# Kernel tuning notes

Measured on AMD Instinct MI355X. Metric: run time of the kernel, lower is better.

Reference implementation:

```python
import jax, jax.numpy as jnp
import numpy as np

IMG = 1024.0
POOL = 7
STRIDES = (4, 8, 16, 32)  # levels P2..P5
STDS = jnp.array([0.1, 0.1, 0.2, 0.2], dtype=jnp.float32)  # RCNN_TARGET_STDS


def delta2bbox(rois, deltas):
    # rois: [N,4] (y1,x1,y2,x2) pixels; deltas: [N,4]
    d = deltas * STDS  # means are zero
    y1, x1, y2, x2 = rois[:, 0], rois[:, 1], rois[:, 2], rois[:, 3]
    h = y2 - y1
    w = x2 - x1
    cy = y1 + 0.5 * h + d[:, 0] * h
    cx = x1 + 0.5 * w + d[:, 1] * w
    h = h * jnp.exp(d[:, 2])
    w = w * jnp.exp(d[:, 3])
    b = jnp.stack([cy - 0.5 * h, cx - 0.5 * w, cy + 0.5 * h, cx + 0.5 * w], axis=1)
    return jnp.clip(b, 0.0, IMG)


def crop_level(feat, rois, stride):
    # feat: [H,W,C]; bilinear 7x7 crop (crop_and_resize style)
    H, W, _ = feat.shape
    s = rois / stride
    grid = (jnp.arange(POOL, dtype=jnp.float32) + 0.5) / POOL
    ys = s[:, 0:1] + grid[None, :] * (s[:, 2:3] - s[:, 0:1])  # [N,7]
    xs = s[:, 1:2] + grid[None, :] * (s[:, 3:4] - s[:, 1:2])  # [N,7]
    y0f = jnp.clip(jnp.floor(ys), 0.0, H - 1)
    x0f = jnp.clip(jnp.floor(xs), 0.0, W - 1)
    y0 = y0f.astype(jnp.int32)
    x0 = x0f.astype(jnp.int32)
    y1 = jnp.minimum(y0 + 1, H - 1)
    x1 = jnp.minimum(x0 + 1, W - 1)
    wy = jnp.clip(ys - y0f, 0.0, 1.0)[:, :, None, None]  # [N,7,1,1]
    wx = jnp.clip(xs - x0f, 0.0, 1.0)[:, None, :, None]  # [N,1,7,1]
    g = lambda yi, xi: feat[yi[:, :, None], xi[:, None, :]]  # [N,7,7,C]
    return (g(y0, x0) * (1 - wy) * (1 - wx) + g(y0, x1) * (1 - wy) * wx
            + g(y1, x0) * wy * (1 - wx) + g(y1, x1) * wy * wx)


def pyramid_roi_align(feats, rois):
    h = rois[:, 2] - rois[:, 0]
    w = rois[:, 3] - rois[:, 1]
    lvl = jnp.floor(4.0 + jnp.log2(jnp.sqrt(jnp.maximum(h * w, 1e-6)) / 224.0))
    lvl = jnp.clip(lvl, 2.0, 5.0).astype(jnp.int32)
    pooled = 0.0
    for i, (feat, stride) in enumerate(zip(feats, STRIDES)):
        mask = (lvl == i + 2).astype(feat.dtype)[:, None, None, None]
        pooled = pooled + crop_level(feat, rois, stride) * mask
    return pooled  # [N,7,7,C]


def bbox_head(pooled, i, fc1_w, fc1_b, fc2_w, fc2_b, cls_w, cls_b, reg_w, reg_b):
    n = pooled.shape[0]
    x = pooled.reshape(n, -1)
    h1 = jax.nn.relu(x @ fc1_w[i] + fc1_b[i])
    h2 = jax.nn.relu(h1 @ fc2_w[i] + fc2_b[i])
    logits = h2 @ cls_w[i] + cls_b[i]
    probs = jax.nn.softmax(logits, axis=-1)
    deltas = h2 @ reg_w[i] + reg_b[i]
    return logits, probs, deltas


def setup_inputs() -> dict:
    key = jax.random.key(0)
    ks = jax.random.split(key, 16)
    d = {}
    for j, (name, shp) in enumerate([("P2", (1, 256, 256, 256)), ("P3", (1, 128, 128, 256)),
                                     ("P4", (1, 64, 64, 256)), ("P5", (1, 32, 32, 256))]):
        d[name] = jax.random.normal(ks[j], shp, dtype=jnp.float32)
    N = 1000
    u = jax.random.uniform(ks[4], (N, 4))
    hh = 16.0 * 2.0 ** (u[:, 0] * 5.0)  # box sizes 16..512 px, spans all pyramid levels
    ww = 16.0 * 2.0 ** (u[:, 1] * 5.0)
    y1 = u[:, 2] * (IMG - hh)
    x1 = u[:, 3] * (IMG - ww)
    d["rois"] = jnp.stack([y1, x1, y1 + hh, x1 + ww], axis=1)
    d["fc1_w"] = jax.random.normal(ks[5], (3, 12544, 1024), dtype=jnp.float32) * 0.01
    d["fc1_b"] = jnp.zeros((3, 1024), jnp.float32)
    d["fc2_w"] = jax.random.normal(ks[6], (3, 1024, 1024), dtype=jnp.float32) * 0.02
    d["fc2_b"] = jnp.zeros((3, 1024), jnp.float32)
    d["cls_w"] = jax.random.normal(ks[7], (3, 1024, 81), dtype=jnp.float32) * 0.02
    d["cls_b"] = jnp.zeros((3, 81), jnp.float32)
    d["reg_w"] = jax.random.normal(ks[8], (3, 1024, 4), dtype=jnp.float32) * 0.01
    d["reg_b"] = jnp.zeros((3, 4), jnp.float32)
    return d


def reference(P2, P3, P4, P5, rois, fc1_w, fc1_b, fc2_w, fc2_b, cls_w, cls_b, reg_w, reg_b):
    feats = [P2[0], P3[0], P4[0], P5[0]]
    params = (fc1_w, fc1_b, fc2_w, fc2_b, cls_w, cls_b, reg_w, reg_b)
    r = rois
    probs3 = None
    pooled = None
    for i in range(3):
        pooled = pyramid_roi_align(feats, r)
        _, probs3, deltas = bbox_head(pooled, i, *params)
        if i < 2:
            r = delta2bbox(r, deltas)
    # test-time ensemble: heads 1 and 2 re-applied to final pooled regions
    _, probs1, _ = bbox_head(pooled, 0, *params)
    _, probs2, _ = bbox_head(pooled, 1, *params)
    return (probs3 + probs1 + probs2) / 3.0
```

## Files before the change

### kernel.cpp

```cpp
#include <hip/hip_runtime.h>


#define BM 128
#define BN 128
#define BK 32
#define K1 12544
#define MPAD 1024
#define NROI 1000

typedef __bf16 bf16_t;
typedef bf16_t bf16x8 __attribute__((ext_vector_type(8)));
typedef float f32x4 __attribute__((ext_vector_type(4)));
typedef float f32x2 __attribute__((ext_vector_type(2)));
typedef unsigned short u16x4 __attribute__((ext_vector_type(4)));
typedef unsigned short u16x2 __attribute__((ext_vector_type(2)));

__device__ __forceinline__ unsigned short f2bf(float x) {
  unsigned u = __float_as_uint(x);
  return (unsigned short)((u + 0x7fffu + ((u >> 16) & 1u)) >> 16);
}
__device__ __forceinline__ float bf2f(unsigned short h) {
  return __uint_as_float(((unsigned)h) << 16);
}

__device__ __forceinline__ void gld_lds16(const void* g, void* l) {
  __builtin_amdgcn_global_load_lds(
      (__attribute__((address_space(1))) void*)g,
      (__attribute__((address_space(3))) void*)l, 16, 0, 0);
}

template <bool SPLIT>
__global__ __launch_bounds__(256, 4)
void gemm_bf16(const unsigned short* __restrict__ Ah,
               const unsigned short* __restrict__ Al,
               long long strideA_head,
               const unsigned short* __restrict__ Bh,
               const unsigned short* __restrict__ Bl,
               long long strideB_head,
               float* __restrict__ Cpart,
               int Nh, int K, int kcSteps)
{
  __shared__ __align__(16) unsigned short sAh[BM * BK];
  __shared__ __align__(16) unsigned short sBh[BN * BK];
  __shared__ __align__(16) unsigned short sAl[SPLIT ? BM * BK : 8];
  __shared__ __align__(16) unsigned short sBl[SPLIT ? BN * BK : 8];

  const int t = threadIdx.x;
  const int ntile = Nh / BN;
  const int bm = blockIdx.x / ntile;
  const int bn = blockIdx.x % ntile;
  const int s = blockIdx.y;
  const int h = blockIdx.z;
  const int H = gridDim.z;

  const unsigned short* Ab = Ah + (size_t)h * strideA_head + (size_t)bm * BM * K;
  const unsigned short* Bb = Bh + (size_t)h * strideB_head + (size_t)bn * BN * K;
  const unsigned short* Alb = SPLIT ? (Al + (size_t)h * strideA_head + (size_t)bm * BM * K) : (const unsigned short*)0;
  const unsigned short* Blb = SPLIT ? (Bl + (size_t)h * strideB_head + (size_t)bn * BN * K) : (const unsigned short*)0;

  int k0 = s * kcSteps * BK;
  int k1 = min(K, k0 + kcSteps * BK);

  const int srow = t >> 2;
  const int gsw = ((t & 3) ^ ((srow >> 1) & 3)) * 8;
  const int lane = t & 63;
  const int wv = t >> 6;
  const int wm = (wv >> 1) * 64;
  const int wn = (wv & 1) * 64;
  const int lr = lane & 15;
  const int q = lane >> 4;
  const int sw = (lr >> 1) & 3;
  const int cA = (q ^ sw) * 8;

  f32x4 acc[4][4];
  const f32x4 z = {0.f, 0.f, 0.f, 0.f};
#pragma unroll
  for (int i = 0; i < 4; ++i)
#pragma unroll
    for (int j = 0; j < 4; ++j) acc[i][j] = z;

  for (int kk = k0; kk < k1; kk += BK) {
#pragma unroll
    for (int j = 0; j < 2; ++j) {
      int row = j * 64 + srow;
      gld_lds16(Ab + (size_t)row * K + kk + gsw, (char*)sAh + j * 4096 + t * 16);
      gld_lds16(Bb + (size_t)row * K + kk + gsw, (char*)sBh + j * 4096 + t * 16);
      if constexpr (SPLIT) {
        gld_lds16(Alb + (size_t)row * K + kk + gsw, (char*)sAl + j * 4096 + t * 16);
        gld_lds16(Blb + (size_t)row * K + kk + gsw, (char*)sBl + j * 4096 + t * 16);
      }
    }
    __syncthreads();

    bf16x8 af[4], bfr[4];
#pragma unroll
    for (int i = 0; i < 4; ++i) af[i] = *(const bf16x8*)&sAh[(wm + i * 16 + lr) * BK + cA];
#pragma unroll
    for (int j = 0; j < 4; ++j) bfr[j] = *(const bf16x8*)&sBh[(wn + j * 16 + lr) * BK + cA];
#pragma unroll
    for (int i = 0; i < 4; ++i)
#pragma unroll
      for (int j = 0; j < 4; ++j)
        acc[i][j] = __builtin_amdgcn_mfma_f32_16x16x32_bf16(af[i], bfr[j], acc[i][j], 0, 0, 0);

    if constexpr (SPLIT) {
      bf16x8 al[4], bl[4];
#pragma unroll
      for (int i = 0; i < 4; ++i) al[i] = *(const bf16x8*)&sAl[(wm + i * 16 + lr) * BK + cA];
#pragma unroll
      for (int j = 0; j < 4; ++j) bl[j] = *(const bf16x8*)&sBl[(wn + j * 16 + lr) * BK + cA];
#pragma unroll
      for (int i = 0; i < 4; ++i)
#pragma unroll
        for (int j = 0; j < 4; ++j) {
          acc[i][j] = __builtin_amdgcn_mfma_f32_16x16x32_bf16(af[i], bl[j], acc[i][j], 0, 0, 0);
          acc[i][j] = __builtin_amdgcn_mfma_f32_16x16x32_bf16(al[i], bfr[j], acc[i][j], 0, 0, 0);
        }
    }
    __syncthreads();
  }

  float* Cb = Cpart + ((size_t)(s * H + h) * MPAD + (size_t)bm * BM) * Nh + (size_t)bn * BN;
#pragma unroll
  for (int i = 0; i < 4; ++i)
#pragma unroll
    for (int j = 0; j < 4; ++j)
#pragma unroll
      for (int r = 0; r < 4; ++r) {
        int m = wm + i * 16 + q * 4 + r;
        int n = wn + j * 16 + lr;
        Cb[(size_t)m * Nh + n] = acc[i][j][r];
      }
}

__global__ __launch_bounds__(256)
void epilogue_kernel(const float* __restrict__ Cpart, int S, int H, int Nh,
                     const float* __restrict__ bias,
                     unsigned short* __restrict__ ohi,
                     unsigned short* __restrict__ olo, int flags)
{
  size_t total = (size_t)H * MPAD * Nh;
  size_t idx = ((size_t)blockIdx.x * 256 + threadIdx.x) * 4;
  if (idx >= total) return;
  int n = (int)(idx % Nh);
  int h = (int)(idx / ((size_t)MPAD * Nh));
  f32x4 v = *(const f32x4*)&bias[(size_t)h * Nh + n];
  for (int s = 0; s < S; ++s) v += *(const f32x4*)&Cpart[(size_t)s * total + idx];
  u16x4 hi, lo;
#pragma unroll
  for (int j = 0; j < 4; ++j) {
    float x = fmaxf(v[j], 0.f);
    hi[j] = f2bf(x);
    lo[j] = f2bf(x - bf2f(hi[j]));
  }
  *(u16x4*)&ohi[idx] = hi;
  if (flags & 4) *(u16x4*)&olo[idx] = lo;
}

__global__ __launch_bounds__(256)
void transpose_convert(const float* __restrict__ W,
                       unsigned short* __restrict__ Thi,
                       unsigned short* __restrict__ Tlo,
                       int K, int N, int loHeads)
{
  __shared__ float tile[32][260];
  int kb = blockIdx.x * 256;
  int nb = blockIdx.y * 32;
  int h = blockIdx.z;
  const float* Wb = W + (size_t)h * K * N + (size_t)kb * N + nb;
  int tn = threadIdx.x & 31;
  int tk = threadIdx.x >> 5;
#pragma unroll
  for (int i = 0; i < 32; ++i) {
    int k = tk + i * 8;
    tile[tn][k] = Wb[(size_t)k * N + tn];
  }
  __syncthreads();
  bool wlo = h < loHeads;
  int l = threadIdx.x & 63;
  int ng = threadIdx.x >> 6;
  size_t ob = (size_t)h * N * K + (size_t)nb * K + kb;
#pragma unroll
  for (int i = 0; i < 8; ++i) {
    int n = ng + i * 4;
    f32x4 v = *(const f32x4*)&tile[n][4 * l];
    u16x4 hi;
#pragma unroll
    for (int j = 0; j < 4; ++j) hi[j] = f2bf(v[j]);
    *(u16x4*)&Thi[ob + (size_t)n * K + 4 * l] = hi;
    if (wlo) {
      u16x4 lo;
#pragma unroll
      for (int j = 0; j < 4; ++j) lo[j] = f2bf(v[j] - bf2f(hi[j]));
      *(u16x4*)&Tlo[ob + (size_t)n * K + 4 * l] = lo;
    }
  }
}

__global__ void transpose_cls(const float* __restrict__ W, unsigned short* __restrict__ T)
{
  int n = blockIdx.x, h = blockIdx.y, t = threadIdx.x;
  size_t ob = ((size_t)h * 128 + n) * 1024;
  if (n < 81) {
    for (int k = t; k < 1024; k += 256)
      T[ob + k] = f2bf(W[((size_t)h * 1024 + k) * 81 + n]);
  } else {
    for (int k = t; k < 1024; k += 256) T[ob + k] = 0;
  }
}

__global__ void roi_align_kernel(const float* __restrict__ rois,
                                 const float* __restrict__ P2, const float* __restrict__ P3,
                                 const float* __restrict__ P4, const float* __restrict__ P5,
                                 unsigned short* __restrict__ phi,
                                 unsigned short* __restrict__ plo, int writeLo)
{
  int m = blockIdx.x;
  int t = threadIdx.x;
  int c = (t & 127) * 2;
  int pg = t >> 7;
  const float* rp = rois + m * 4;
  float y1 = rp[0], x1 = rp[1], y2 = rp[2], x2 = rp[3];
  float hh = y2 - y1, ww = x2 - x1;
  float a = sqrtf(fmaxf(hh * ww, 1e-6f)) / 224.0f;
  float lvl = floorf(4.0f + log2f(a));
  lvl = fminf(fmaxf(lvl, 2.0f), 5.0f);
  int i = (int)lvl - 2;
  const float* f = (i == 0) ? P2 : (i == 1) ? P3 : (i == 2) ? P4 : P5;
  int H = 256 >> i;
  float stride = (float)(4 << i);
  float sy1 = y1 / stride, sx1 = x1 / stride;
  float dy = y2 / stride - sy1, dx = x2 / stride - sx1;
  size_t base = (size_t)m * K1 + c;
  for (int p = pg; p < 49; p += 2) {
    int py = p / 7, px = p % 7;
    float ys = sy1 + ((py + 0.5f) / 7.0f) * dy;
    float xs = sx1 + ((px + 0.5f) / 7.0f) * dx;
    float y0f = fminf(fmaxf(floorf(ys), 0.0f), (float)(H - 1));
    float x0f = fminf(fmaxf(floorf(xs), 0.0f), (float)(H - 1));
    int y0 = (int)y0f, x0 = (int)x0f;
    int y1i = min(y0 + 1, H - 1), x1i = min(x0 + 1, H - 1);
    float wy = fminf(fmaxf(ys - y0f, 0.0f), 1.0f);
    float wx = fminf(fmaxf(xs - x0f, 0.0f), 1.0f);
    f32x2 v00 = *(const f32x2*)(f + ((size_t)y0 * H + x0) * 256 + c);
    f32x2 v01 = *(const f32x2*)(f + ((size_t)y0 * H + x1i) * 256 + c);
    f32x2 v10 = *(const f32x2*)(f + ((size_t)y1i * H + x0) * 256 + c);
    f32x2 v11 = *(const f32x2*)(f + ((size_t)y1i * H + x1i) * 256 + c);
    float w00 = (1.f - wy) * (1.f - wx), w01 = (1.f - wy) * wx;
    float w10 = wy * (1.f - wx), w11 = wy * wx;
    f32x2 v = v00 * w00 + v01 * w01 + v10 * w10 + v11 * w11;
    u16x2 hi;
    hi[0] = f2bf(v[0]); hi[1] = f2bf(v[1]);
    *(u16x2*)&phi[base + p * 256] = hi;
    if (writeLo) {
      u16x2 lo;
      lo[0] = f2bf(v[0] - bf2f(hi[0]));
      lo[1] = f2bf(v[1] - bf2f(hi[1]));
      *(u16x2*)&plo[base + p * 256] = lo;
    }
  }
}

__global__ void reg_delta_kernel(const float* __restrict__ Cpart, int S,
                                 const float* __restrict__ fb,
                                 const float* __restrict__ rw, const float* __restrict__ rb,
                                 const float* __restrict__ rin, float* __restrict__ rout)
{
  int m = blockIdx.x, t = threadIdx.x;
  float s0 = 0, s1 = 0, s2 = 0, s3 = 0;
  for (int n = t; n < 1024; n += 256) {
    float v = fb[n];
    for (int s = 0; s < S; ++s) v += Cpart[((size_t)s * 1024 + m) * 1024 + n];
    v = fmaxf(v, 0.f);
    const float* w = rw + (size_t)n * 4;
    s0 += v * w[0]; s1 += v * w[1]; s2 += v * w[2]; s3 += v * w[3];
  }
#pragma unroll
  for (int o = 32; o > 0; o >>= 1) {
    s0 += __shfl_xor(s0, o, 64);
    s1 += __shfl_xor(s1, o, 64);
    s2 += __shfl_xor(s2, o, 64);
    s3 += __shfl_xor(s3, o, 64);
  }
  __shared__ float part[4][4];
  int w = t >> 6;
  if ((t & 63) == 0) { part[w][0] = s0; part[w][1] = s1; part[w][2] = s2; part[w][3] = s3; }
  __syncthreads();
  if (t == 0) {
    float d0 = (part[0][0] + part[1][0] + part[2][0] + part[3][0] + rb[0]) * 0.1f;
    float d1 = (part[0][1] + part[1][1] + part[2][1] + part[3][1] + rb[1]) * 0.1f;
    float d2 = (part[0][2] + part[1][2] + part[2][2] + part[3][2] + rb[2]) * 0.2f;
    float d3 = (part[0][3] + part[1][3] + part[2][3] + part[3][3] + rb[3]) * 0.2f;
    const float* r = rin + m * 4;
    float y1 = r[0], x1 = r[1], y2 = r[2], x2 = r[3];
    float h = y2 - y1, wd = x2 - x1;
    float cy = y1 + 0.5f * h + d0 * h;
    float cx = x1 + 0.5f * wd + d1 * wd;
    float nh = h * expf(d2);
    float nw = wd * expf(d3);
    float* ro = rout + m * 4;
    ro[0] = fminf(fmaxf(cy - 0.5f * nh, 0.f), 1024.f);
    ro[1] = fminf(fmaxf(cx - 0.5f * nw, 0.f), 1024.f);
    ro[2] = fminf(fmaxf(cy + 0.5f * nh, 0.f), 1024.f);
    ro[3] = fminf(fmaxf(cx + 0.5f * nw, 0.f), 1024.f);
  }
}

__global__ void softmax_avg_kernel(const float* __restrict__ Cpart, int S,
                                   const float* __restrict__ cls_b,
                                   float* __restrict__ out)
{
  int m = blockIdx.x, t = threadIdx.x;
  __shared__ float sh[128];
  float pacc = 0.0f;
  for (int h = 0; h < 3; ++h) {
    float x = -3.0e38f;
    if (t < 81) {
      x = cls_b[h * 81 + t];
      for (int s = 0; s < S; ++s)
        x += Cpart[((size_t)(s * 3 + h) * 1024 + m) * 128 + t];
    }
    sh[t] = x; __syncthreads();
    for (int o = 64; o > 0; o >>= 1) { if (t < o) sh[t] = fmaxf(sh[t], sh[t + o]); __syncthreads(); }
    float mx = sh[0]; __syncthreads();
    float e = (t < 81) ? expf(x - mx) : 0.0f;
    sh[t] = e; __syncthreads();
    for (int o = 64; o > 0; o >>= 1) { if (t < o) sh[t] += sh[t + o]; __syncthreads(); }
    float sum = sh[0]; __syncthreads();
    pacc += e / sum;
  }
  if (t < 81) out[(size_t)m * 81 + t] = pacc / 3.0f;
}

extern "C" void kernel_launch(void* const* d_in, const int* in_sizes, int n_in,
                              void* d_out, int out_size, void* d_ws, size_t ws_size,
                              hipStream_t stream)
{
  const float* P2 = (const float*)d_in[0];
  const float* P3 = (const float*)d_in[1];
  const float* P4 = (const float*)d_in[2];
  const float* P5 = (const float*)d_in[3];
  const float* rois = (const float*)d_in[4];
  const float* fc1_w = (const float*)d_in[5];
  const float* fc1_b = (const float*)d_in[6];
  const float* fc2_w = (const float*)d_in[7];
  const float* fc2_b = (const float*)d_in[8];
  const float* cls_w = (const float*)d_in[9];
  const float* cls_b = (const float*)d_in[10];
  const float* reg_w = (const float*)d_in[11];
  const float* reg_b = (const float*)d_in[12];
  float* out = (float*)d_out;

  char* ws = (char*)d_ws;
  size_t off = 0;
  auto alloc = [&](size_t b) -> char* {
    char* p = ws + off;
    off = (off + b + 255) & ~(size_t)255;
    return p;
  };
  unsigned short* w1t_hi = (unsigned short*)alloc(3ull * 1024 * K1 * 2);
  unsigned short* w2t_hi = (unsigned short*)alloc(3ull * 1024 * 1024 * 2);
  unsigned short* w2t_lo = (unsigned short*)alloc(2ull * 1024 * 1024 * 2);
  unsigned short* w3t    = (unsigned short*)alloc(3ull * 128 * 1024 * 2);
  unsigned short* phi    = (unsigned short*)alloc((size_t)MPAD * K1 * 2);
  unsigned short* plo    = (unsigned short*)alloc((size_t)MPAD * K1 * 2);
  unsigned short* h1_hi  = (unsigned short*)alloc(3ull * MPAD * 1024 * 2);
  unsigned short* h1_lo  = (unsigned short*)alloc((size_t)MPAD * 1024 * 2);
  unsigned short* h2_hi  = (unsigned short*)alloc(3ull * MPAD * 1024 * 2);
  float* r1              = (float*)alloc(16384);
  float* r2              = (float*)alloc(16384);
  const size_t w1lo_bytes = 2ull * 1024 * K1 * 2;
  unsigned short* w1t_lo = (unsigned short*)alloc(w1lo_bytes);

  const size_t SLAB = (size_t)MPAD * 1024 * 4;
  size_t tail = (ws_size > off) ? (ws_size - off) : 0;

  int S01 = (int)(tail / SLAB);
  if (S01 > 8) S01 = 8;
  if (S01 < 1) S01 = 1;
  float* cpart01 = (float*)(ws + off);
  const int S2 = 4;
  float* cpart2 = (float*)w1t_lo;

  const int fc1Steps01 = (392 + S01 - 1) / S01;
  const int fc2Steps01 = (32 + S01 - 1) / S01;
  const int fc1Steps2 = (392 + S2 - 1) / S2;

  const long long hs1 = (long long)1024 * K1;
  const long long hs2 = (long long)1024 * 1024;

  dim3 b256(256);

  hipLaunchKernelGGL(transpose_convert, dim3(K1 / 256, 32, 3), b256, 0, stream,
                     fc1_w, w1t_hi, w1t_lo, K1, 1024, 2);
  hipLaunchKernelGGL(transpose_convert, dim3(4, 32, 3), b256, 0, stream,
                     fc2_w, w2t_hi, w2t_lo, 1024, 1024, 2);
  hipLaunchKernelGGL(transpose_cls, dim3(128, 3), b256, 0, stream, cls_w, w3t);
  hipMemsetAsync(phi + (size_t)NROI * K1, 0, (size_t)(MPAD - NROI) * K1 * 2, stream);
  hipMemsetAsync(plo + (size_t)NROI * K1, 0, (size_t)(MPAD - NROI) * K1 * 2, stream);

  for (int st = 0; st < 2; ++st) {
    const float* rin = (st == 0) ? rois : r1;
    float* rout = (st == 0) ? r1 : r2;
    hipLaunchKernelGGL(roi_align_kernel, dim3(NROI), b256, 0, stream,
                       rin, P2, P3, P4, P5, phi, plo, 1);
    hipLaunchKernelGGL((gemm_bf16<true>), dim3(64, S01, 1), b256, 0, stream,
                       phi, plo, 0LL,
                       w1t_hi + (size_t)st * hs1, w1t_lo + (size_t)st * hs1, 0LL,
                       cpart01, 1024, K1, fc1Steps01);
    hipLaunchKernelGGL(epilogue_kernel, dim3(1024), b256, 0, stream,
                       cpart01, S01, 1, 1024, fc1_b + st * 1024,
                       h1_hi, h1_lo, 4);
    hipLaunchKernelGGL((gemm_bf16<true>), dim3(64, S01, 1), b256, 0, stream,
                       h1_hi, h1_lo, 0LL,
                       w2t_hi + (size_t)st * hs2, w2t_lo + (size_t)st * hs2, 0LL,
                       cpart01, 1024, 1024, fc2Steps01);
    hipLaunchKernelGGL(reg_delta_kernel, dim3(NROI), b256, 0, stream,
                       cpart01, S01, fc2_b + st * 1024,
                       reg_w + (size_t)st * 1024 * 4, reg_b + st * 4,
                       rin, rout);
  }

  hipLaunchKernelGGL(roi_align_kernel, dim3(NROI), b256, 0, stream,
                     r2, P2, P3, P4, P5, phi, plo, 0);
  hipLaunchKernelGGL((gemm_bf16<false>), dim3(64, S2, 3), b256, 0, stream,
                     phi, (const unsigned short*)0, 0LL,
                     w1t_hi, (const unsigned short*)0, hs1,
                     cpart2, 1024, K1, fc1Steps2);
  hipLaunchKernelGGL(epilogue_kernel, dim3(3072), b256, 0, stream,
                     cpart2, S2, 3, 1024, fc1_b,
                     h1_hi, (unsigned short*)0, 0);
  hipLaunchKernelGGL((gemm_bf16<false>), dim3(64, S2, 3), b256, 0, stream,
                     h1_hi, (const unsigned short*)0, hs2,
                     w2t_hi, (const unsigned short*)0, hs2,
                     cpart2, 1024, 1024, (32 + S2 - 1) / S2);
  hipLaunchKernelGGL(epilogue_kernel, dim3(3072), b256, 0, stream,
                     cpart2, S2, 3, 1024, fc2_b,
                     h2_hi, (unsigned short*)0, 0);
  hipLaunchKernelGGL((gemm_bf16<false>), dim3(8, 8, 3), b256, 0, stream,
                     h2_hi, (const unsigned short*)0, hs2,
                     w3t, (const unsigned short*)0, (long long)128 * 1024,
                     cpart2, 128, 1024, 4);
  hipLaunchKernelGGL(softmax_avg_kernel, dim3(NROI), dim3(128), 0, stream,
                     cpart2, 8, cls_b, out);
}
```

Measured before the change: 844.8 us.

## Use 256x256 ping-pong MFMA GEMM for final-stage three-head fc1

Replaces the final three-head fc1 GEMM with a new 256x256-tile, 512-thread kernel. It treats the three heads as one N=3072 problem, uses swizzled LDS double buffering with direct global-to-LDS loads, phased MFMA scheduling and priority hints, and sets split-K from the available workspace. A matching epilogue scatters results back into per-head layout. The ROI-align kernel is also widened to 4-channel vector loads. The goals are more data reuse per tile, less launch and grid overhead, and better memory efficiency. In exchange it needs 128KB of LDS per block and relies on the cpart2 workspace being large enough.

```diff
diff --git a/kernel.cpp b/kernel.cpp
--- a/kernel.cpp
+++ b/kernel.cpp
@@ -133,6 +133,148 @@
       }
 }
 
+#define DS_A(XB, MH) do { \
+    rA[0][0]=lda_f(XB,(MH)*4+0,0); rA[0][1]=lda_f(XB,(MH)*4+0,1); \
+    rA[1][0]=lda_f(XB,(MH)*4+1,0); rA[1][1]=lda_f(XB,(MH)*4+1,1); \
+    rA[2][0]=lda_f(XB,(MH)*4+2,0); rA[2][1]=lda_f(XB,(MH)*4+2,1); \
+    rA[3][0]=lda_f(XB,(MH)*4+3,0); rA[3][1]=lda_f(XB,(MH)*4+3,1); } while(0)
+
+#define DS_B(XB, NH) do { \
+    rB[(NH)*2+0][0]=ldb_f(XB,(NH)*2+0,0); rB[(NH)*2+0][1]=ldb_f(XB,(NH)*2+0,1); \
+    rB[(NH)*2+1][0]=ldb_f(XB,(NH)*2+1,0); rB[(NH)*2+1][1]=ldb_f(XB,(NH)*2+1,1); } while(0)
+
+#define MFMA_Q(MH, NH) do { \
+  _Pragma("unroll") \
+  for (int ii = 0; ii < 4; ++ii) { \
+    _Pragma("unroll") \
+    for (int jj = 0; jj < 2; ++jj) { \
+      acc[(MH)*4+ii][(NH)*2+jj] = __builtin_amdgcn_mfma_f32_16x16x32_bf16(rA[ii][0], rB[(NH)*2+jj][0], acc[(MH)*4+ii][(NH)*2+jj], 0, 0, 0); \
+      acc[(MH)*4+ii][(NH)*2+jj] = __builtin_amdgcn_mfma_f32_16x16x32_bf16(rA[ii][1], rB[(NH)*2+jj][1], acc[(MH)*4+ii][(NH)*2+jj], 0, 0, 0); \
+    } } } while(0)
+
+#define PHASE_SYNC() do { \
+  __builtin_amdgcn_s_barrier(); \
+  asm volatile("s_waitcnt lgkmcnt(0)" ::: "memory"); \
+  __builtin_amdgcn_sched_barrier(0); } while(0)
+
+#define PHASE_END() do { \
+  __builtin_amdgcn_s_setprio(0); \
+  __builtin_amdgcn_s_barrier(); } while(0)
+
+__global__ __launch_bounds__(512, 2)
+void gemm256_bf16(const unsigned short* __restrict__ A,
+                  const unsigned short* __restrict__ B,
+                  float* __restrict__ Cpart,
+                  int Ntot, int K, int tilesTotal)
+{
+  extern __shared__ char lds[];
+  const int t = threadIdx.x;
+  const int ntile = Ntot >> 8;
+  const int bm = blockIdx.x / ntile;
+  const int bn = blockIdx.x % ntile;
+  const int s = blockIdx.y;
+  const int S = gridDim.y;
+  const int qp = tilesTotal / S, rp = tilesTotal % S;
+  const int t0 = s * qp + (s < rp ? s : rp);
+  const int np = qp + (s < rp ? 1 : 0);
+
+  const unsigned short* Ab = A + (size_t)bm * 256 * K;
+  const unsigned short* Bb = B + (size_t)bn * 256 * K;
+
+  const int srow = t >> 3;
+  const int sgrp = ((t & 7) ^ (srow & 7)) << 3;
+
+  const int lane = t & 63;
+  const int wv = t >> 6;
+  const int wm = (wv >> 2) << 7;
+  const int wn = (wv & 3) << 6;
+  const int lr = lane & 15;
+  const int q = lane >> 4;
+
+  f32x4 acc[8][4];
+  const f32x4 z = {0.f, 0.f, 0.f, 0.f};
+#pragma unroll
+  for (int i = 0; i < 8; ++i)
+#pragma unroll
+    for (int j = 0; j < 4; ++j) acc[i][j] = z;
+
+  bf16x8 rA[4][2], rB[4][2];
+
+  auto stage_tile = [&](int xbuf, int kt) {
+    const size_t col = ((size_t)(t0 + kt) << 6) + sgrp;
+#pragma unroll
+    for (int u = 0; u < 4; ++u) {
+      const unsigned short* src = (u < 2) ? Ab : Bb;
+      const int rbase = ((u & 1) << 7) + srow;
+      char* dst = lds + xbuf * 65536 + ((u & 2) << 14) + ((u & 1) << 14) + t * 16;
+      gld_lds16(src + (size_t)rbase * K + col, dst);
+      gld_lds16(src + (size_t)(rbase + 64) * K + col, dst + 8192);
+    }
+  };
+
+  auto lda_f = [&](int xbuf, int i, int ks) -> bf16x8 {
+    const int row = wm + (i << 4) + lr;
+    const int pg = (ks * 4 + q) ^ (row & 7);
+    return *(const bf16x8*)(lds + xbuf * 65536 + row * 128 + pg * 16);
+  };
+  auto ldb_f = [&](int xbuf, int j, int ks) -> bf16x8 {
+    const int row = wn + (j << 4) + lr;
+    const int pg = (ks * 4 + q) ^ (row & 7);
+    return *(const bf16x8*)(lds + xbuf * 65536 + 32768 + row * 128 + pg * 16);
+  };
+
+  stage_tile(0, 0);
+  if (np > 1) {
+    stage_tile(1, 1);
+    asm volatile("s_waitcnt vmcnt(8)" ::: "memory");
+  } else {
+    asm volatile("s_waitcnt vmcnt(0)" ::: "memory");
+  }
+  __builtin_amdgcn_s_barrier();
+
+  for (int i = 0; i < np; ++i) {
+    const int buf = i & 1;
+    const bool st = (i + 2 < np);
+    DS_A(buf, 0);
+    DS_B(buf, 0);
+    PHASE_SYNC();
+    __builtin_amdgcn_s_setprio(1);
+    MFMA_Q(0, 0);
+    PHASE_END();
+    DS_B(buf, 1);
+    PHASE_SYNC();
+    __builtin_amdgcn_s_setprio(1);
+    MFMA_Q(0, 1);
+    PHASE_END();
+    DS_A(buf, 1);
+    PHASE_SYNC();
+    __builtin_amdgcn_s_setprio(1);
+    MFMA_Q(1, 0);
+    PHASE_END();
+    if (st) {
+      stage_tile(buf, i + 2);
+      asm volatile("s_waitcnt vmcnt(8)" ::: "memory");
+    } else {
+      asm volatile("s_waitcnt vmcnt(0)" ::: "memory");
+    }
+    __builtin_amdgcn_s_barrier();
+    __builtin_amdgcn_sched_barrier(0);
+    __builtin_amdgcn_s_setprio(1);
+    MFMA_Q(1, 1);
+    __builtin_amdgcn_s_setprio(0);
+  }
+
+  float* Cb = Cpart + (size_t)s * MPAD * Ntot +
+              (size_t)(bm * 256 + wm) * Ntot + bn * 256 + wn;
+#pragma unroll
+  for (int i = 0; i < 8; ++i)
+#pragma unroll
+    for (int j = 0; j < 4; ++j)
+#pragma unroll
+      for (int r = 0; r < 4; ++r)
+        Cb[(size_t)(i * 16 + q * 4 + r) * Ntot + j * 16 + lr] = acc[i][j][r];
+}
+
 __global__ __launch_bounds__(256)
 void epilogue_kernel(const float* __restrict__ Cpart, int S, int H, int Nh,
                      const float* __restrict__ bias,
@@ -158,6 +300,25 @@
 }
 
 __global__ __launch_bounds__(256)
+void epilogue_fc1_s2(const float* __restrict__ Cpart, int S,
+                     const float* __restrict__ bias,
+                     unsigned short* __restrict__ ohi)
+{
+  const size_t total = (size_t)MPAD * 3072;
+  size_t idx = ((size_t)blockIdx.x * 256 + threadIdx.x) * 4;
+  if (idx >= total) return;
+  int n = (int)(idx % 3072);
+  int m = (int)(idx / 3072);
+  f32x4 v = *(const f32x4*)&bias[n];
+  for (int s = 0; s < S; ++s) v += *(const f32x4*)&Cpart[(size_t)s * total + idx];
+  u16x4 hi;
+#pragma unroll
+  for (int j = 0; j < 4; ++j) hi[j] = f2bf(fmaxf(v[j], 0.f));
+  int h = n >> 10;
+  *(u16x4*)&ohi[((size_t)h * MPAD + m) * 1024 + (n & 1023)] = hi;
+}
+
+__global__ __launch_bounds__(256)
 void transpose_convert(const float* __restrict__ W,
                        unsigned short* __restrict__ Thi,
                        unsigned short* __restrict__ Tlo,
@@ -217,8 +378,8 @@
 {
   int m = blockIdx.x;
   int t = threadIdx.x;
-  int c = (t & 127) * 2;
-  int pg = t >> 7;
+  int c = (t & 63) * 4;
+  int pg = t >> 6;
   const float* rp = rois + m * 4;
   float y1 = rp[0], x1 = rp[1], y2 = rp[2], x2 = rp[3];
   float hh = y2 - y1, ww = x2 - x1;
@@ -232,7 +393,7 @@
   float sy1 = y1 / stride, sx1 = x1 / stride;
   float dy = y2 / stride - sy1, dx = x2 / stride - sx1;
   size_t base = (size_t)m * K1 + c;
-  for (int p = pg; p < 49; p += 2) {
+  for (int p = pg; p < 49; p += 4) {
     int py = p / 7, px = p % 7;
     float ys = sy1 + ((py + 0.5f) / 7.0f) * dy;
     float xs = sx1 + ((px + 0.5f) / 7.0f) * dx;
@@ -242,21 +403,23 @@
     int y1i = min(y0 + 1, H - 1), x1i = min(x0 + 1, H - 1);
     float wy = fminf(fmaxf(ys - y0f, 0.0f), 1.0f);
     float wx = fminf(fmaxf(xs - x0f, 0.0f), 1.0f);
-    f32x2 v00 = *(const f32x2*)(f + ((size_t)y0 * H + x0) * 256 + c);
-    f32x2 v01 = *(const f32x2*)(f + ((size_t)y0 * H + x1i) * 256 + c);
-    f32x2 v10 = *(const f32x2*)(f + ((size_t)y1i * H + x0) * 256 + c);
-    f32x2 v11 = *(const f32x2*)(f + ((size_t)y1i * H + x1i) * 256 + c);
+    f32x4 v00 = *(const f32x4*)(f + ((size_t)y0 * H + x0) * 256 + c);
+    f32x4 v01 = *(const f32x4*)(f + ((size_t)y0 * H + x1i) * 256 + c);
+    f32x4 v10 = *(const f32x4*)(f + ((size_t)y1i * H + x0) * 256 + c);
+    f32x4 v11 = *(const f32x4*)(f + ((size_t)y1i * H + x1i) * 256 + c);
     float w00 = (1.f - wy) * (1.f - wx), w01 = (1.f - wy) * wx;
     float w10 = wy * (1.f - wx), w11 = wy * wx;
-    f32x2 v = v00 * w00 + v01 * w01 + v10 * w10 + v11 * w11;
-    u16x2 hi;
-    hi[0] = f2bf(v[0]); hi[1] = f2bf(v[1]);
-    *(u16x2*)&phi[base + p * 256] = hi;
+    f32x4 v = v00 * w00 + v01 * w01 + v10 * w10 + v11 * w11;
+    u16x4 hi;
+#pragma unroll
+    for (int j = 0; j < 4; ++j) hi[j] = f2bf(v[j]);
+    *(u16x4*)&phi[base + p * 256] = hi;
     if (writeLo) {
-      u16x2 lo;
-      lo[0] = f2bf(v[0] - bf2f(hi[0]));
-      lo[1] = f2bf(v[1] - bf2f(hi[1]));
-      *(u16x2*)&plo[base + p * 256] = lo;
+      u16x4 lo;
+#pragma unroll
+      for (int j = 0; j < 4; ++j) lo[j] = f2bf(v[j] - bf2f(hi[j]));
+      *(u16x2*)&plo[base + p * 256] = *(u16x2*)&lo;
+      *(u16x2*)&plo[base + p * 256 + 2] = *((u16x2*)&lo + 1);
     }
   }
 }
@@ -384,7 +547,6 @@
 
   const int fc1Steps01 = (392 + S01 - 1) / S01;
   const int fc2Steps01 = (32 + S01 - 1) / S01;
-  const int fc1Steps2 = (392 + S2 - 1) / S2;
 
   const long long hs1 = (long long)1024 * K1;
   const long long hs2 = (long long)1024 * 1024;
@@ -423,13 +585,16 @@
 
   hipLaunchKernelGGL(roi_align_kernel, dim3(NROI), b256, 0, stream,
                      r2, P2, P3, P4, P5, phi, plo, 0);
-  hipLaunchKernelGGL((gemm_bf16<false>), dim3(64, S2, 3), b256, 0, stream,
-                     phi, (const unsigned short*)0, 0LL,
-                     w1t_hi, (const unsigned short*)0, hs1,
-                     cpart2, 1024, K1, fc1Steps2);
-  hipLaunchKernelGGL(epilogue_kernel, dim3(3072), b256, 0, stream,
-                     cpart2, S2, 3, 1024, fc1_b,
-                     h1_hi, (unsigned short*)0, 0);
+  {
+    const size_t SLAB3 = (size_t)MPAD * 3072 * 4;
+    size_t availC2 = ws_size - (size_t)((char*)w1t_lo - ws);
+    int S2f = 5;
+    while (S2f > 1 && (size_t)S2f * SLAB3 > availC2) --S2f;
+    hipLaunchKernelGGL(gemm256_bf16, dim3(48, S2f), dim3(512), 131072, stream,
+                       phi, w1t_hi, cpart2, 3072, K1, 196);
+    hipLaunchKernelGGL(epilogue_fc1_s2, dim3(3072), b256, 0, stream,
+                       cpart2, S2f, fc1_b, h1_hi);
+  }
   hipLaunchKernelGGL((gemm_bf16<false>), dim3(64, S2, 3), b256, 0, stream,
                      h1_hi, (const unsigned short*)0, hs2,
                      w2t_hi, (const unsigned short*)0, hs2,
```

Result: faster. 824.4 us (-2.4%).
